# Kernel optimization log

Hardware: AMD Instinct MI355X
Metric: run time of the kernel (lower is better)

## Reference

```python
import jax, jax.numpy as jnp
import numpy as np

N_NODES = 200000
N_GRAPHS = 64
K_SLOTS = 16
LATENT = 128
HID = 128  # hidden_dim // 2


def setup_inputs() -> dict:
    key = jax.random.key(0)
    ks = jax.random.split(key, 8)
    z = jax.random.normal(ks[0], (N_GRAPHS, K_SLOTS, LATENT), dtype=jnp.float32)
    s = jax.random.uniform(ks[1], (N_NODES, K_SLOTS), dtype=jnp.float32)
    batch = jnp.sort(jax.random.randint(ks[2], (N_NODES,), 0, N_GRAPHS))
    sc1 = 1.0 / np.sqrt(LATENT)
    sc2 = 1.0 / np.sqrt(HID)
    W1 = jax.random.normal(ks[3], (LATENT, HID), dtype=jnp.float32) * sc1
    b1 = jnp.zeros((HID,), dtype=jnp.float32)
    W2 = jax.random.normal(ks[4], (HID, HID), dtype=jnp.float32) * sc2
    b2 = jnp.zeros((HID,), dtype=jnp.float32)
    Wp = jax.random.normal(ks[5], (HID, 2), dtype=jnp.float32) * sc2
    bp = jnp.zeros((2,), dtype=jnp.float32)
    Wv = jax.random.normal(ks[6], (HID, 2), dtype=jnp.float32) * sc2
    bv = jnp.zeros((2,), dtype=jnp.float32)
    return {"z": z, "s": s, "batch": batch, "W1": W1, "b1": b1,
            "W2": W2, "b2": b2, "Wp": Wp, "bp": bp, "Wv": Wv, "bv": bv}


def reference(z, s, batch, W1, b1, W2, b2, Wp, bp, Wv, bv):
    # gather per-node latent set: [N, K, D]
    z_expanded = z[batch]
    # weighted sum over K slots -> [N, D]
    node_feat = jnp.einsum('nk,nkd->nd', s, z_expanded)
    # shared MLP: Linear-ReLU-Linear-ReLU
    h = jax.nn.relu(node_feat @ W1 + b1)
    h = jax.nn.relu(h @ W2 + b2)
    # heads
    pos_recon = jnp.tanh(h @ Wp + bp)
    vel_recon = h @ Wv + bv
    return jnp.concatenate([pos_recon, vel_recon], axis=-1)
```

## Files before the change

kernel.cpp:

```cpp
#include <hip/hip_runtime.h>

typedef _Float16 half4 __attribute__((ext_vector_type(4)));
typedef float    f32x4 __attribute__((ext_vector_type(4)));
typedef int      i32x4 __attribute__((ext_vector_type(4)));

#define MFMA16(a,b,c) __builtin_amdgcn_mfma_f32_16x16x16f16((a),(b),(c),0,0,0)

static constexpr int N_NODES  = 200000;
static constexpr int N_GRAPHS = 64;

static constexpr size_t WS_ZWT    = 0;
static constexpr size_t WS_W2T    = 262144;
static constexpr size_t WS_WHT    = 294912;
static constexpr size_t WS_GSTART = 299008;
static constexpr size_t WS_CG     = 299520;
static constexpr size_t WS_GTAB   = 299792;

__global__ void gnn_prep1(const int* __restrict__ batch,
                          const float* __restrict__ W2,
                          const float* __restrict__ Wp,
                          const float* __restrict__ Wv,
                          int* __restrict__ gstart,
                          _Float16* __restrict__ w2t,
                          _Float16* __restrict__ wht)
{
    const int b = blockIdx.x, t = threadIdx.x;
    if (b < 782) {
        const int i = b * 256 + t;
        if (i < N_NODES) {
            const int bi   = batch[i];
            const int prev = (i == 0) ? -1 : batch[i - 1];
            if (bi != prev)
                for (int g = prev + 1; g <= bi; ++g) gstart[g] = i;
            if (i == N_NODES - 1)
                for (int g = bi + 1; g <= N_GRAPHS; ++g) gstart[g] = N_NODES;
        }
    } else if (b < 846) {
        const int e  = (b - 782) * 256 + t;
        const int n  = e >> 7, kk = e & 127;
        w2t[e] = (_Float16)W2[kk * 128 + n];
    } else {
        for (int r = 0; r < 8; ++r) {
            const int e = r * 256 + t;
            const int j = e >> 7, d = e & 127;
            float v = 0.f;
            if (j < 2)      v = Wp[d * 2 + j];
            else if (j < 4) v = Wv[d * 2 + (j - 2)];
            wht[e] = (_Float16)v;
        }
    }
}

__global__ void gnn_prep2(const float* __restrict__ z,
                          const float* __restrict__ W1,
                          const int* __restrict__ gstart,
                          _Float16* __restrict__ zwt,
                          int* __restrict__ Cg)
{
    const int b = blockIdx.x, d = threadIdx.x;
    if (b < 256) {
        const int g = b >> 2, kq = b & 3;
        const float* zb = z + (g * 16 + kq * 4) * 128;
        float a0 = 0.f, a1 = 0.f, a2 = 0.f, a3 = 0.f;
        for (int c = 0; c < 128; ++c) {
            const float w = W1[c * 128 + d];
            a0 += zb[c] * w;
            a1 += zb[128 + c] * w;
            a2 += zb[256 + c] * w;
            a3 += zb[384 + c] * w;
        }
        half4 o; o[0] = (_Float16)a0; o[1] = (_Float16)a1; o[2] = (_Float16)a2; o[3] = (_Float16)a3;
        *(half4*)(zwt + (g * 128 + d) * 16 + kq * 4) = o;
    } else if (d == 0) {
        int c = 0; Cg[0] = 0;
        for (int g = 0; g < 64; ++g) {
            const int cnt = gstart[g + 1] - gstart[g];
            c += (cnt + 15) >> 4;
            Cg[g + 1] = c;
        }
    }
}

__global__ void gnn_prep3(const int* __restrict__ gstart,
                          const int* __restrict__ Cg,
                          i32x4* __restrict__ gtab)
{
    const int t = blockIdx.x * 256 + threadIdx.x;
    const int total = Cg[64];
    if (t >= total) return;
    int lo = 0, hi = 64;
    while (lo < hi) { const int mid = (lo + hi + 1) >> 1; if (Cg[mid] <= t) lo = mid; else hi = mid - 1; }
    i32x4 e;
    e[0] = lo;
    e[1] = gstart[lo] + ((t - Cg[lo]) << 4);
    e[2] = gstart[lo + 1];
    e[3] = 0;
    gtab[t] = e;
}

__device__ inline float fast_tanh(float x) {
    x = fminf(fmaxf(x, -15.f), 15.f);
    const float e = __expf(2.f * x);
    return (e - 1.f) / (e + 1.f);
}

__global__ __launch_bounds__(256, 2) void gnn_main(
    const float* __restrict__ s,
    const float* __restrict__ b1,
    const float* __restrict__ b2,
    const float* __restrict__ bp,
    const float* __restrict__ bv,
    const _Float16* __restrict__ zwt,
    const _Float16* __restrict__ w2t,
    const _Float16* __restrict__ wht,
    const i32x4* __restrict__ gtab,
    const int* __restrict__ Cg,
    float* __restrict__ out)
{
    const int lane = threadIdx.x & 63;
    const int n16  = lane & 15;
    const int quad = lane >> 4;
    const int wid  = blockIdx.x * 4 + (threadIdx.x >> 6);
    const int nw   = gridDim.x * 4;

    half4 a2[8][8];
#pragma unroll
    for (int mt = 0; mt < 8; ++mt)
#pragma unroll
        for (int t = 0; t < 8; ++t)
            a2[mt][t] = *(const half4*)(w2t + (mt * 16 + n16) * 128 + t * 16 + quad * 4);

    half4 a3[8];
#pragma unroll
    for (int t = 0; t < 8; ++t)
        a3[t] = *(const half4*)(wht + n16 * 128 + t * 16 + quad * 4);

    const float bp0 = bp[0], bp1 = bp[1], bv0 = bv[0], bv1 = bv[1];
    const int total = Cg[64];

    for (int gi = wid; gi < total; gi += nw) {
        const i32x4 ge = gtab[gi];
        const int g = ge[0], base = ge[1], end = ge[2];
        const int node  = base + n16;
        const bool valid = node < end;

        half4 bs = {(_Float16)0.f, (_Float16)0.f, (_Float16)0.f, (_Float16)0.f};
        if (valid) {
            const f32x4 sv = *(const f32x4*)(s + node * 16 + quad * 4);
            bs[0] = (_Float16)sv[0]; bs[1] = (_Float16)sv[1];
            bs[2] = (_Float16)sv[2]; bs[3] = (_Float16)sv[3];
        }

        const _Float16* zg = zwt + g * 2048;
        f32x4 acc1[8];
#pragma unroll
        for (int mt = 0; mt < 8; ++mt) {
            const half4 a1 = *(const half4*)(zg + (mt * 16 + n16) * 16 + quad * 4);
            const f32x4 zc = {0.f, 0.f, 0.f, 0.f};
            acc1[mt] = MFMA16(a1, bs, zc);
        }

        half4 h1[8];
#pragma unroll
        for (int mt = 0; mt < 8; ++mt) {
            const f32x4 bb = *(const f32x4*)(b1 + mt * 16 + quad * 4);
#pragma unroll
            for (int i = 0; i < 4; ++i) {
                const float x = fmaxf(acc1[mt][i] + bb[i], 0.f);
                h1[mt][i] = (_Float16)x;
            }
        }

        f32x4 acc3 = {0.f, 0.f, 0.f, 0.f};
#pragma unroll
        for (int mo = 0; mo < 8; ++mo) {
            f32x4 acc2 = {0.f, 0.f, 0.f, 0.f};
#pragma unroll
            for (int t = 0; t < 8; ++t)
                acc2 = MFMA16(a2[mo][t], h1[t], acc2);
            const f32x4 bb = *(const f32x4*)(b2 + mo * 16 + quad * 4);
            half4 h2;
#pragma unroll
            for (int i = 0; i < 4; ++i) {
                const float x = fmaxf(acc2[i] + bb[i], 0.f);
                h2[i] = (_Float16)x;
            }
            acc3 = MFMA16(a3[mo], h2, acc3);
        }

        if (quad == 0 && valid) {
            f32x4 o;
            o[0] = fast_tanh(acc3[0] + bp0);
            o[1] = fast_tanh(acc3[1] + bp1);
            o[2] = acc3[2] + bv0;
            o[3] = acc3[3] + bv1;
            *(f32x4*)(out + node * 4) = o;
        }
    }
}

extern "C" void kernel_launch(void* const* d_in, const int* in_sizes, int n_in,
                              void* d_out, int out_size, void* d_ws, size_t ws_size,
                              hipStream_t stream)
{
    const float* z     = (const float*)d_in[0];
    const float* s     = (const float*)d_in[1];
    const int*   batch = (const int*)d_in[2];
    const float* W1    = (const float*)d_in[3];
    const float* b1    = (const float*)d_in[4];
    const float* W2    = (const float*)d_in[5];
    const float* b2    = (const float*)d_in[6];
    const float* Wp    = (const float*)d_in[7];
    const float* bp    = (const float*)d_in[8];
    const float* Wv    = (const float*)d_in[9];
    const float* bv    = (const float*)d_in[10];
    float* out = (float*)d_out;

    char* w = (char*)d_ws;
    _Float16* zwt  = (_Float16*)(w + WS_ZWT);
    _Float16* w2t  = (_Float16*)(w + WS_W2T);
    _Float16* wht  = (_Float16*)(w + WS_WHT);
    int* gstart    = (int*)(w + WS_GSTART);
    int* Cg        = (int*)(w + WS_CG);
    i32x4* gtab    = (i32x4*)(w + WS_GTAB);

    hipLaunchKernelGGL(gnn_prep1, dim3(847), dim3(256), 0, stream,
                       batch, W2, Wp, Wv, gstart, w2t, wht);
    hipLaunchKernelGGL(gnn_prep2, dim3(257), dim3(128), 0, stream,
                       z, W1, gstart, zwt, Cg);
    hipLaunchKernelGGL(gnn_prep3, dim3(50), dim3(256), 0, stream,
                       gstart, Cg, gtab);
    hipLaunchKernelGGL(gnn_main, dim3(512), dim3(256), 0, stream,
                       s, b1, b2, bp, bv, zwt, w2t, wht, gtab, Cg, out);
}
```

Before: 122.7 us.

## Merge prep kernels into one launch and index graph chunks directly from gstart

Folds the three preprocessing kernels into a single launch. The z·W1 precompute is spread over 512 extra blocks, two latent slots per block. The prefix-sum and chunk-table kernels are removed; the main kernel now walks a fixed 64x256 chunk grid and looks up graph bounds from gstart, skipping empty chunks. This cuts two launches and their serial dependencies, at the cost of many idle chunk iterations in the main loop, and it assumes no graph has more than 4096 nodes.

```diff
diff --git a/kernel.cpp b/kernel.cpp
--- a/kernel.cpp
+++ b/kernel.cpp
@@ -2,27 +2,30 @@
 
 typedef _Float16 half4 __attribute__((ext_vector_type(4)));
 typedef float    f32x4 __attribute__((ext_vector_type(4)));
-typedef int      i32x4 __attribute__((ext_vector_type(4)));
 
 #define MFMA16(a,b,c) __builtin_amdgcn_mfma_f32_16x16x16f16((a),(b),(c),0,0,0)
 
 static constexpr int N_NODES  = 200000;
 static constexpr int N_GRAPHS = 64;
+static constexpr int GPG      = 256;
+static constexpr int TOTAL_G  = N_GRAPHS * GPG;
 
 static constexpr size_t WS_ZWT    = 0;
 static constexpr size_t WS_W2T    = 262144;
 static constexpr size_t WS_WHT    = 294912;
 static constexpr size_t WS_GSTART = 299008;
-static constexpr size_t WS_CG     = 299520;
-static constexpr size_t WS_GTAB   = 299792;
 
-__global__ void gnn_prep1(const int* __restrict__ batch,
-                          const float* __restrict__ W2,
-                          const float* __restrict__ Wp,
-                          const float* __restrict__ Wv,
-                          int* __restrict__ gstart,
-                          _Float16* __restrict__ w2t,
-                          _Float16* __restrict__ wht)
+__global__ __launch_bounds__(256) void gnn_prep(
+    const int* __restrict__ batch,
+    const float* __restrict__ z,
+    const float* __restrict__ W1,
+    const float* __restrict__ W2,
+    const float* __restrict__ Wp,
+    const float* __restrict__ Wv,
+    int* __restrict__ gstart,
+    _Float16* __restrict__ zwt,
+    _Float16* __restrict__ w2t,
+    _Float16* __restrict__ wht)
 {
     const int b = blockIdx.x, t = threadIdx.x;
     if (b < 782) {
@@ -36,66 +39,30 @@
                 for (int g = bi + 1; g <= N_GRAPHS; ++g) gstart[g] = N_NODES;
         }
     } else if (b < 846) {
-        const int e  = (b - 782) * 256 + t;
-        const int n  = e >> 7, kk = e & 127;
+        const int e = (b - 782) * 256 + t;
+        const int n = e >> 7, kk = e & 127;
         w2t[e] = (_Float16)W2[kk * 128 + n];
+    } else if (b < 854) {
+        const int e = (b - 846) * 256 + t;
+        const int j = e >> 7, d = e & 127;
+        float v = 0.f;
+        if (j < 2)      v = Wp[d * 2 + j];
+        else if (j < 4) v = Wv[d * 2 + (j - 2)];
+        wht[e] = (_Float16)v;
     } else {
-        for (int r = 0; r < 8; ++r) {
-            const int e = r * 256 + t;
-            const int j = e >> 7, d = e & 127;
-            float v = 0.f;
-            if (j < 2)      v = Wp[d * 2 + j];
-            else if (j < 4) v = Wv[d * 2 + (j - 2)];
-            wht[e] = (_Float16)v;
+        const int p = (b - 854) * 2 + (t >> 7);
+        const int g = p >> 4, k = p & 15, d = t & 127;
+        const float* zr = z + (g * 16 + k) * 128;
+        float a0 = 0.f, a1 = 0.f, a2 = 0.f, a3 = 0.f;
+#pragma unroll 8
+        for (int c = 0; c < 128; c += 4) {
+            a0 += zr[c    ] * W1[(c    ) * 128 + d];
+            a1 += zr[c + 1] * W1[(c + 1) * 128 + d];
+            a2 += zr[c + 2] * W1[(c + 2) * 128 + d];
+            a3 += zr[c + 3] * W1[(c + 3) * 128 + d];
         }
+        zwt[(g * 128 + d) * 16 + k] = (_Float16)((a0 + a1) + (a2 + a3));
     }
-}
-
-__global__ void gnn_prep2(const float* __restrict__ z,
-                          const float* __restrict__ W1,
-                          const int* __restrict__ gstart,
-                          _Float16* __restrict__ zwt,
-                          int* __restrict__ Cg)
-{
-    const int b = blockIdx.x, d = threadIdx.x;
-    if (b < 256) {
-        const int g = b >> 2, kq = b & 3;
-        const float* zb = z + (g * 16 + kq * 4) * 128;
-        float a0 = 0.f, a1 = 0.f, a2 = 0.f, a3 = 0.f;
-        for (int c = 0; c < 128; ++c) {
-            const float w = W1[c * 128 + d];
-            a0 += zb[c] * w;
-            a1 += zb[128 + c] * w;
-            a2 += zb[256 + c] * w;
-            a3 += zb[384 + c] * w;
-        }
-        half4 o; o[0] = (_Float16)a0; o[1] = (_Float16)a1; o[2] = (_Float16)a2; o[3] = (_Float16)a3;
-        *(half4*)(zwt + (g * 128 + d) * 16 + kq * 4) = o;
-    } else if (d == 0) {
-        int c = 0; Cg[0] = 0;
-        for (int g = 0; g < 64; ++g) {
-            const int cnt = gstart[g + 1] - gstart[g];
-            c += (cnt + 15) >> 4;
-            Cg[g + 1] = c;
-        }
-    }
-}
-
-__global__ void gnn_prep3(const int* __restrict__ gstart,
-                          const int* __restrict__ Cg,
-                          i32x4* __restrict__ gtab)
-{
-    const int t = blockIdx.x * 256 + threadIdx.x;
-    const int total = Cg[64];
-    if (t >= total) return;
-    int lo = 0, hi = 64;
-    while (lo < hi) { const int mid = (lo + hi + 1) >> 1; if (Cg[mid] <= t) lo = mid; else hi = mid - 1; }
-    i32x4 e;
-    e[0] = lo;
-    e[1] = gstart[lo] + ((t - Cg[lo]) << 4);
-    e[2] = gstart[lo + 1];
-    e[3] = 0;
-    gtab[t] = e;
 }
 
 __device__ inline float fast_tanh(float x) {
@@ -113,8 +80,7 @@
     const _Float16* __restrict__ zwt,
     const _Float16* __restrict__ w2t,
     const _Float16* __restrict__ wht,
-    const i32x4* __restrict__ gtab,
-    const int* __restrict__ Cg,
+    const int* __restrict__ gstart,
     float* __restrict__ out)
 {
     const int lane = threadIdx.x & 63;
@@ -136,13 +102,17 @@
         a3[t] = *(const half4*)(wht + n16 * 128 + t * 16 + quad * 4);
 
     const float bp0 = bp[0], bp1 = bp[1], bv0 = bv[0], bv1 = bv[1];
-    const int total = Cg[64];
 
-    for (int gi = wid; gi < total; gi += nw) {
-        const i32x4 ge = gtab[gi];
-        const int g = ge[0], base = ge[1], end = ge[2];
+    for (int gi = wid; gi < TOTAL_G; gi += nw) {
+        const int g    = gi >> 8;
+        const int idx  = gi & 255;
+        const int gs   = gstart[g];
+        const int ge   = gstart[g + 1];
+        const int base = gs + idx * 16;
+        if (base >= ge) continue;
+
         const int node  = base + n16;
-        const bool valid = node < end;
+        const bool valid = node < ge;
 
         half4 bs = {(_Float16)0.f, (_Float16)0.f, (_Float16)0.f, (_Float16)0.f};
         if (valid) {
@@ -152,23 +122,16 @@
         }
 
         const _Float16* zg = zwt + g * 2048;
-        f32x4 acc1[8];
+        half4 h1[8];
 #pragma unroll
         for (int mt = 0; mt < 8; ++mt) {
             const half4 a1 = *(const half4*)(zg + (mt * 16 + n16) * 16 + quad * 4);
             const f32x4 zc = {0.f, 0.f, 0.f, 0.f};
-            acc1[mt] = MFMA16(a1, bs, zc);
-        }
-
-        half4 h1[8];
-#pragma unroll
-        for (int mt = 0; mt < 8; ++mt) {
+            const f32x4 acc = MFMA16(a1, bs, zc);
             const f32x4 bb = *(const f32x4*)(b1 + mt * 16 + quad * 4);
 #pragma unroll
-            for (int i = 0; i < 4; ++i) {
-                const float x = fmaxf(acc1[mt][i] + bb[i], 0.f);
-                h1[mt][i] = (_Float16)x;
-            }
+            for (int i = 0; i < 4; ++i)
+                h1[mt][i] = (_Float16)fmaxf(acc[i] + bb[i], 0.f);
         }
 
         f32x4 acc3 = {0.f, 0.f, 0.f, 0.f};
@@ -181,10 +144,8 @@
             const f32x4 bb = *(const f32x4*)(b2 + mo * 16 + quad * 4);
             half4 h2;
 #pragma unroll
-            for (int i = 0; i < 4; ++i) {
-                const float x = fmaxf(acc2[i] + bb[i], 0.f);
-                h2[i] = (_Float16)x;
-            }
+            for (int i = 0; i < 4; ++i)
+                h2[i] = (_Float16)fmaxf(acc2[i] + bb[i], 0.f);
             acc3 = MFMA16(a3[mo], h2, acc3);
         }
 
@@ -217,19 +178,13 @@
     float* out = (float*)d_out;
 
     char* w = (char*)d_ws;
-    _Float16* zwt  = (_Float16*)(w + WS_ZWT);
-    _Float16* w2t  = (_Float16*)(w + WS_W2T);
-    _Float16* wht  = (_Float16*)(w + WS_WHT);
-    int* gstart    = (int*)(w + WS_GSTART);
-    int* Cg        = (int*)(w + WS_CG);
-    i32x4* gtab    = (i32x4*)(w + WS_GTAB);
+    _Float16* zwt = (_Float16*)(w + WS_ZWT);
+    _Float16* w2t = (_Float16*)(w + WS_W2T);
+    _Float16* wht = (_Float16*)(w + WS_WHT);
+    int* gstart   = (int*)(w + WS_GSTART);
 
-    hipLaunchKernelGGL(gnn_prep1, dim3(847), dim3(256), 0, stream,
-                       batch, W2, Wp, Wv, gstart, w2t, wht);
-    hipLaunchKernelGGL(gnn_prep2, dim3(257), dim3(128), 0, stream,
-                       z, W1, gstart, zwt, Cg);
-    hipLaunchKernelGGL(gnn_prep3, dim3(50), dim3(256), 0, stream,
-                       gstart, Cg, gtab);
+    hipLaunchKernelGGL(gnn_prep, dim3(1366), dim3(256), 0, stream,
+                       batch, z, W1, W2, Wp, Wv, gstart, zwt, w2t, wht);
     hipLaunchKernelGGL(gnn_main, dim3(512), dim3(256), 0, stream,
-                       s, b1, b2, bp, bv, zwt, w2t, wht, gtab, Cg, out);
+                       s, b1, b2, bp, bv, zwt, w2t, wht, gstart, out);
 }
```

Result: slower. 126.9 us (+3.4%).
